# Kernel tuning notes

Measured on AMD Instinct MI355X. Metric: run time of the kernel, lower is better.

The kernel has to match this reference:

```python
import jax, jax.numpy as jnp
import numpy as np

NUM_HEADS = 8
NUM_LANDMARKS = 64


def setup_inputs() -> dict:
    key = jax.random.key(0)
    k1, k2, k3, k4, k5 = jax.random.split(key, 5)
    B, N, C = 4, 8192, 512
    x = jax.random.normal(k1, (B, N, C), dtype=jnp.float32)
    qkv_w = jax.random.normal(k2, (C, 3 * C), dtype=jnp.float32) * (C ** -0.5)
    qkv_b = jax.random.normal(k3, (3 * C,), dtype=jnp.float32) * 0.01
    proj_w = jax.random.normal(k4, (C, C), dtype=jnp.float32) * (C ** -0.5)
    proj_b = jax.random.normal(k5, (C,), dtype=jnp.float32) * 0.01
    return {"x": x, "qkv_w": qkv_w, "qkv_b": qkv_b, "proj_w": proj_w, "proj_b": proj_b}


def reference(x, qkv_w, qkv_b, proj_w, proj_b):
    B, N, C = x.shape
    H = NUM_HEADS
    D = C // H
    m = min(NUM_LANDMARKS, N)
    scale = D ** -0.5

    # qkv projection -> [3, B, H, N, D]
    qkv = (x @ qkv_w + qkv_b).reshape(B, N, 3, H, D).transpose(2, 0, 3, 1, 4)
    q, k, v = qkv[0], qkv[1], qkv[2]

    if m >= N:
        attn = jax.nn.softmax(jnp.einsum('bhnd,bhkd->bhnk', q, k) * scale, axis=-1)
        out = attn @ v  # [B,H,N,D]
    else:
        # landmark indices: linspace(0, N-1, m).long()
        idx = jnp.linspace(0, N - 1, m).astype(jnp.int32)
        q_l = q[:, :, idx]  # [B,H,m,D]
        k_l = k[:, :, idx]  # [B,H,m,D]
        kernel_1 = jax.nn.softmax(jnp.einsum('bhnd,bhmd->bhnm', q, k_l) * scale, axis=-1)  # [B,H,N,m]
        kernel_2 = jax.nn.softmax(jnp.einsum('bhmd,bhkd->bhmk', q_l, k_l) * scale, axis=-1)  # [B,H,m,m]
        kernel_3 = jax.nn.softmax(jnp.einsum('bhmd,bhnd->bhmn', q_l, k) * scale, axis=-1)  # [B,H,m,N]
        k2_inv = jnp.linalg.pinv(kernel_2)  # [B,H,m,m]
        # fuse right-to-left to keep intermediates small: [B,H,m,D]
        out = kernel_1 @ (k2_inv @ (kernel_3 @ v))  # [B,H,N,D]

    out = out.transpose(0, 2, 1, 3).reshape(B, N, C)
    return out @ proj_w + proj_b
```

## Files before the change

### kernel.cpp

```cpp
#include <hip/hip_runtime.h>
#include <stdint.h>

using bf16x8 = __attribute__((ext_vector_type(8))) short;
using bf16x8_t = __attribute__((ext_vector_type(8))) __bf16;
using f32x4  = __attribute__((ext_vector_type(4))) float;
typedef unsigned short u16;
typedef unsigned int   u32;

#define DEVI static __device__ __forceinline__

typedef u32 __attribute__((address_space(1))) gu32;
typedef u32 __attribute__((address_space(3))) lu32;

DEVI u16 f2b(float f) {
  union { float f; u32 u; } v; v.f = f;
  u32 r = v.u + 0x7FFFu + ((v.u >> 16) & 1u);
  return (u16)(r >> 16);
}

DEVI f32x4 mfma16(bf16x8 a, bf16x8 b, f32x4 c) {
  return __builtin_amdgcn_mfma_f32_16x16x32_bf16(
      __builtin_bit_cast(bf16x8_t, a), __builtin_bit_cast(bf16x8_t, b), c, 0, 0, 0);
}

DEVI void gload16(const void* g, void* l) {
  __builtin_amdgcn_global_load_lds((const gu32*)(uintptr_t)g,
                                   (lu32*)(u32)(uintptr_t)l, 16, 0, 0);
}

DEVI int swz64(int row, int ch) { return row*64 + ((ch ^ (row & 7)) << 3); }

#define VMCNT0 asm volatile("s_waitcnt vmcnt(0)" ::: "memory")
#define LGKM0  asm volatile("s_waitcnt lgkmcnt(0)" ::: "memory")

__global__ void __launch_bounds__(256) k_cast_x(const float4* __restrict__ xin,
                                                uint4* __restrict__ xo, int n8) {
  int i = blockIdx.x * 256 + threadIdx.x;
  if (i >= n8) return;
  float4 a = xin[2*i], b = xin[2*i+1];
  uint4 o;
  o.x = ((u32)f2b(a.y) << 16) | f2b(a.x);
  o.y = ((u32)f2b(a.w) << 16) | f2b(a.z);
  o.z = ((u32)f2b(b.y) << 16) | f2b(b.x);
  o.w = ((u32)f2b(b.w) << 16) | f2b(b.z);
  xo[i] = o;
}

__global__ void __launch_bounds__(256) k_tcast(const float* __restrict__ w,
                                               u16* __restrict__ wt, int R, int Cc) {
  int o = blockIdx.x * 256 + threadIdx.x;
  if (o >= R * Cc) return;
  int c = o % R, j = o / R;
  wt[o] = f2b(w[(size_t)c * Cc + j]);
}

__global__ void __launch_bounds__(256) k_lmk(
    const float* __restrict__ x, const float* __restrict__ w,
    const float* __restrict__ bias, float* __restrict__ qlf,
    float* __restrict__ klf, u16* __restrict__ qlb, u16* __restrict__ klb) {
  __shared__ __align__(16) float xr[512];
  const int t = threadIdx.x;
  const int b = blockIdx.x >> 6, i = blockIdx.x & 63;
  const int idx = (i * 8191) / 63;
  const float4* xg = (const float4*)(x + ((size_t)b*8192 + idx)*512);
  if (t < 128) ((float4*)xr)[t] = xg[t];
  __syncthreads();

  const int o0 = t << 2;
  float4 acc = *(const float4*)(bias + o0);
  const float* wp = w + o0;
  #pragma unroll 8
  for (int c = 0; c < 512; ++c) {
    const float xv = xr[c];
    const float4 wv = *(const float4*)(wp + (size_t)c*1536);
    acc.x = fmaf(xv, wv.x, acc.x); acc.y = fmaf(xv, wv.y, acc.y);
    acc.z = fmaf(xv, wv.z, acc.z); acc.w = fmaf(xv, wv.w, acc.w);
  }

  const int h = (o0 >> 6) & 7, d = o0 & 63;
  const size_t ofs = ((size_t)(b*8 + h)*64 + i)*64 + d;
  ushort4 pk;
  pk.x = f2b(acc.x); pk.y = f2b(acc.y); pk.z = f2b(acc.z); pk.w = f2b(acc.w);
  if (o0 < 512) { *(float4*)(qlf + ofs) = acc; *(ushort4*)(qlb + ofs) = pk; }
  else          { *(float4*)(klf + ofs) = acc; *(ushort4*)(klb + ofs) = pk; }
}

template <int MODE>
__global__ void __launch_bounds__(256) k_gemm(
    const u16* __restrict__ A, const u16* __restrict__ Bt,
    const float* __restrict__ bias, int K, int ntn,
    u16* __restrict__ qdst, u16* __restrict__ kdst, u16* __restrict__ vtdst,
    float* __restrict__ fout, int Nout) {
  __shared__ __align__(16) u16 As[128*64];
  __shared__ __align__(16) u16 Bs[128*64];
  const int t = threadIdx.x;
  const int cpx = gridDim.x >> 3;
  const int wgid = (blockIdx.x & 7) * cpx + (blockIdx.x >> 3);
  const int tn = wgid % ntn, tm = wgid / ntn;
  const int m0 = tm << 7, n0 = tn << 7;
  const int w = t >> 6, l = t & 63;
  const int wr = (w >> 1) << 6, wc = (w & 1) << 6;
  const int lhi = l >> 4, llo = l & 15;

  f32x4 acc[4][4];
  #pragma unroll
  for (int i = 0; i < 4; ++i)
    #pragma unroll
    for (int j = 0; j < 4; ++j) acc[i][j] = f32x4{0.f,0.f,0.f,0.f};

  const int csw = (((t & 7) ^ ((t >> 3) & 7)) << 3);
  const u16* ga = A  + (size_t)(m0 + (t >> 3)) * K + csw;
  const u16* gb = Bt + (size_t)(n0 + (t >> 3)) * K + csw;
  u16* lA = As + (w << 9);
  u16* lB = Bs + (w << 9);

  for (int kt = 0; kt < K; kt += 64) {
    __syncthreads();
    #pragma unroll
    for (int i = 0; i < 4; ++i) {
      gload16(ga + (size_t)(i*32)*K + kt, lA + i*2048);
      gload16(gb + (size_t)(i*32)*K + kt, lB + i*2048);
    }
    VMCNT0;
    __syncthreads();
    #pragma unroll
    for (int kko = 0; kko < 64; kko += 32) {
      const int kc = kko >> 3;
      bf16x8 av[4], bv[4];
      #pragma unroll
      for (int mi = 0; mi < 4; ++mi)
        av[mi] = *(const bf16x8*)(As + swz64(wr + mi*16 + llo, kc + lhi));
      #pragma unroll
      for (int ni = 0; ni < 4; ++ni)
        bv[ni] = *(const bf16x8*)(Bs + swz64(wc + ni*16 + llo, kc + lhi));
      #pragma unroll
      for (int mi = 0; mi < 4; ++mi)
        #pragma unroll
        for (int ni = 0; ni < 4; ++ni)
          acc[mi][ni] = mfma16(av[mi], bv[ni], acc[mi][ni]);
    }
  }

  #pragma unroll
  for (int ni = 0; ni < 4; ++ni) {
    const int gcol = n0 + wc + ni*16 + llo;
    const float bvv = bias[gcol];
    if (MODE == 0) {
      const int tt = gcol >> 9, h = (gcol >> 6) & 7, d = gcol & 63;
      #pragma unroll
      for (int mi = 0; mi < 4; ++mi) {
        const int grow = m0 + wr + mi*16 + (lhi << 2);
        const int b = grow >> 13, n = grow & 8191;
        const size_t bh = (size_t)(b*8 + h);
        if (tt == 2) {
          ushort4 pk;
          pk.x = f2b(acc[mi][ni][0] + bvv); pk.y = f2b(acc[mi][ni][1] + bvv);
          pk.z = f2b(acc[mi][ni][2] + bvv); pk.w = f2b(acc[mi][ni][3] + bvv);
          *(ushort4*)(vtdst + (bh*64 + d)*8192 + n) = pk;
        } else {
          u16* dst = (tt == 0 ? qdst : kdst) + (bh*8192 + n)*64 + d;
          #pragma unroll
          for (int r = 0; r < 4; ++r) dst[(size_t)r*64] = f2b(acc[mi][ni][r] + bvv);
        }
      }
    } else {
      #pragma unroll
      for (int mi = 0; mi < 4; ++mi) {
        const int grow = m0 + wr + mi*16 + (lhi << 2);
        #pragma unroll
        for (int r = 0; r < 4; ++r)
          fout[(size_t)(grow + r)*Nout + gcol] = acc[mi][ni][r] + bvv;
      }
    }
  }
}

__global__ void __launch_bounds__(256) k_flash3(
    const u16* __restrict__ qlb, const u16* __restrict__ kmat,
    const u16* __restrict__ vt, float* __restrict__ num_part,
    float* __restrict__ den_part) {
  __shared__ __align__(16) u16 QL[64*64];
  __shared__ __align__(16) u16 KT[4][64*64];
  __shared__ __align__(16) u16 VT[4][64*64];
  __shared__ __align__(16) u16 PL[4][64*64];
  const int t = threadIdx.x, w = t >> 6, l = t & 63;
  const int bh = blockIdx.x >> 3, split = blockIdx.x & 7;
  const int lhi = l >> 4, llo = l & 15;
  const int csw = ((l & 7) ^ (l >> 3)) << 3;

  #pragma unroll
  for (int i = 0; i < 2; ++i)
    gload16(qlb + (size_t)bh*4096 + (size_t)((i*256 + (t & ~7)) << 3)
                + (((t & 7) ^ ((t >> 3) & 7)) << 3),
            QL + i*2048 + (w << 9));
  VMCNT0;
  __syncthreads();

  f32x4 oacc[4][4];
  float dacc[4][4];
  #pragma unroll
  for (int a = 0; a < 4; ++a)
    #pragma unroll
    for (int bq = 0; bq < 4; ++bq) { oacc[a][bq] = f32x4{0.f,0.f,0.f,0.f}; dacc[a][bq] = 0.f; }

  const int nb = split << 10;
  u16* lk = KT[w]; u16* lv = VT[w]; u16* lp = PL[w];
  for (int j = 0; j < 4; ++j) {
    const int n0 = nb + ((w + 4*j) << 6);
    const u16* gk = kmat + ((size_t)bh*8192 + n0 + (l >> 3))*64 + csw;
    const u16* gv = vt   + ((size_t)bh*64 + (l >> 3))*8192 + n0 + csw;
    asm volatile("" ::: "memory");
    LGKM0;
    #pragma unroll
    for (int i = 0; i < 8; ++i) {
      gload16(gk + (size_t)(i*8)*64, lk + i*512);
      gload16(gv + (size_t)(i*8)*8192, lv + i*512);
    }
    VMCNT0;

    f32x4 s[4][4];
    #pragma unroll
    for (int qi = 0; qi < 4; ++qi)
      #pragma unroll
      for (int nj = 0; nj < 4; ++nj) s[qi][nj] = f32x4{0.f,0.f,0.f,0.f};
    #pragma unroll
    for (int kko = 0; kko < 64; kko += 32) {
      const int kc = kko >> 3;
      bf16x8 av[4], bv[4];
      #pragma unroll
      for (int qi = 0; qi < 4; ++qi)
        av[qi] = *(const bf16x8*)(QL + swz64(qi*16 + llo, kc + lhi));
      #pragma unroll
      for (int nj = 0; nj < 4; ++nj)
        bv[nj] = *(const bf16x8*)(lk + swz64(nj*16 + llo, kc + lhi));
      #pragma unroll
      for (int qi = 0; qi < 4; ++qi)
        #pragma unroll
        for (int nj = 0; nj < 4; ++nj)
          s[qi][nj] = mfma16(av[qi], bv[nj], s[qi][nj]);
    }
    #pragma unroll
    for (int qi = 0; qi < 4; ++qi) {
      float rs[4] = {0.f, 0.f, 0.f, 0.f};
      #pragma unroll
      for (int nj = 0; nj < 4; ++nj)
        #pragma unroll
        for (int r = 0; r < 4; ++r) {
          float p = __expf(s[qi][nj][r] * 0.125f);
          rs[r] += p;
          const int prow = qi*16 + lhi*4 + r, pcol = nj*16 + llo;
          lp[swz64(prow, pcol >> 3) + (pcol & 7)] = f2b(p);
        }
      #pragma unroll
      for (int r = 0; r < 4; ++r) {
        float v = rs[r];
        v += __shfl_xor(v, 1); v += __shfl_xor(v, 2);
        v += __shfl_xor(v, 4); v += __shfl_xor(v, 8);
        dacc[qi][r] += v;
      }
    }
    LGKM0;
    #pragma unroll
    for (int kko = 0; kko < 64; kko += 32) {
      const int kc = kko >> 3;
      bf16x8 pa[4], vb[4];
      #pragma unroll
      for (int qi = 0; qi < 4; ++qi)
        pa[qi] = *(const bf16x8*)(lp + swz64(qi*16 + llo, kc + lhi));
      #pragma unroll
      for (int dj = 0; dj < 4; ++dj)
        vb[dj] = *(const bf16x8*)(lv + swz64(dj*16 + llo, kc + lhi));
      #pragma unroll
      for (int qi = 0; qi < 4; ++qi)
        #pragma unroll
        for (int dj = 0; dj < 4; ++dj)
          oacc[qi][dj] = mfma16(pa[qi], vb[dj], oacc[qi][dj]);
    }
  }
  const int sw = (split << 2) + w;
  float* np = num_part + ((size_t)bh*32 + sw)*4096;
  #pragma unroll
  for (int qi = 0; qi < 4; ++qi)
    #pragma unroll
    for (int dj = 0; dj < 4; ++dj)
      #pragma unroll
      for (int r = 0; r < 4; ++r)
        np[(qi*16 + lhi*4 + r)*64 + dj*16 + llo] = oacc[qi][dj][r];
  if (llo == 0) {
    float* dp = den_part + ((size_t)bh*32 + sw)*64;
    #pragma unroll
    for (int qi = 0; qi < 4; ++qi)
      #pragma unroll
      for (int r = 0; r < 4; ++r)
        dp[qi*16 + lhi*4 + r] = dacc[qi][r];
  }
}

__global__ void __launch_bounds__(256) k_t1(
    const float* __restrict__ num_part, const float* __restrict__ den_part,
    float* __restrict__ t1g) {
  const int t = threadIdx.x;
  const int bh = blockIdx.x >> 2, ch = blockIdx.x & 3;
  const int f = ch*256 + t;
  const int m = f >> 4;
  const float4* ng = (const float4*)num_part + (size_t)bh*32*1024;
  float4 acc = {0.f, 0.f, 0.f, 0.f};
  float ds = 0.f;
  for (int s = 0; s < 32; ++s) {
    float4 v = ng[(size_t)s*1024 + f];
    acc.x += v.x; acc.y += v.y; acc.z += v.z; acc.w += v.w;
    ds += den_part[((size_t)bh*32 + s)*64 + m];
  }
  float r = 1.f / ds;
  acc.x *= r; acc.y *= r; acc.z *= r; acc.w *= r;
  ((float4*)t1g)[(size_t)bh*1024 + f] = acc;
}

__global__ void __launch_bounds__(256) k_inv(
    const float* __restrict__ qlf, const float* __restrict__ klf,
    float* __restrict__ invg) {
  __shared__ __align__(16) float A[64*132];
  __shared__ __align__(16) float QL[64*68], KL[64*68];
  __shared__ int pivcol[64];
  __shared__ int piv_s;
  const int t = threadIdx.x;
  const int bh = blockIdx.x;
  const int i4 = t >> 2, jc = t & 3;
  float4* QL4 = (float4*)QL;
  float4* KL4 = (float4*)KL;
  float4* A4  = (float4*)A;

  const float4* qg = (const float4*)(qlf + (size_t)bh*4096);
  const float4* kg = (const float4*)(klf + (size_t)bh*4096);
  #pragma unroll
  for (int k = 0; k < 4; ++k) {
    int g = k*256 + t, row = g >> 4, c4 = g & 15;
    QL4[row*17 + c4] = qg[g];
    KL4[row*17 + c4] = kg[g];
  }
  __syncthreads();

  {
    float4 qreg[16];
    #pragma unroll
    for (int q4 = 0; q4 < 16; ++q4) qreg[q4] = QL4[i4*17 + q4];
    #pragma unroll
    for (int jj = 0; jj < 16; ++jj) {
      int j = jc*16 + jj;
      float acc = 0.f;
      #pragma unroll
      for (int q4 = 0; q4 < 16; ++q4) {
        float4 kv = KL4[j*17 + q4];
        acc = fmaf(qreg[q4].x, kv.x, acc); acc = fmaf(qreg[q4].y, kv.y, acc);
        acc = fmaf(qreg[q4].z, kv.z, acc); acc = fmaf(qreg[q4].w, kv.w, acc);
      }
      A[i4*132 + j] = acc * 0.125f;
    }
  }
  {
    float z[16]; float m = -1e30f;
    #pragma unroll
    for (int jj = 0; jj < 16; ++jj) { z[jj] = A[i4*132 + jc*16 + jj]; m = fmaxf(m, z[jj]); }
    m = fmaxf(m, __shfl_xor(m, 1)); m = fmaxf(m, __shfl_xor(m, 2));
    float s = 0.f;
    #pragma unroll
    for (int jj = 0; jj < 16; ++jj) { z[jj] = __expf(z[jj] - m); s += z[jj]; }
    s += __shfl_xor(s, 1); s += __shfl_xor(s, 2);
    float rinv = 1.f / s;
    #pragma unroll
    for (int jj = 0; jj < 16; ++jj) {
      int j = jc*16 + jj;
      A[i4*132 + j] = z[jj] * rinv;
      A[i4*132 + 64 + j] = (j == i4) ? 1.f : 0.f;
    }
  }
  __syncthreads();

  const int r = i4, q = jc;
  int used = 0;
  for (int c = 0; c < 64; ++c) {
    if (t < 64) {
      float val = used ? -1.f : fabsf(A[t*132 + c]);
      int idx = t;
      #pragma unroll
      for (int mk = 1; mk < 64; mk <<= 1) {
        float ov = __shfl_xor(val, mk);
        int oi = __shfl_xor(idx, mk);
        int take = (ov > val) || (ov == val && oi < idx);
        val = take ? ov : val;
        idx = take ? oi : idx;
      }
      if (t == idx) { used = 1; pivcol[t] = c; }
      if (t == 0) piv_s = idx;
    }
    __syncthreads();
    const int p = piv_s;
    if (r != p) {
      const float coef = -A[r*132 + c] / A[p*132 + c];
      const float4* Ap = A4 + p*33 + q*8;
      float4* Ar = A4 + r*33 + q*8;
      #pragma unroll
      for (int i = 0; i < 8; ++i) {
        float4 a = Ar[i], pv = Ap[i];
        a.x = fmaf(coef, pv.x, a.x); a.y = fmaf(coef, pv.y, a.y);
        a.z = fmaf(coef, pv.z, a.z); a.w = fmaf(coef, pv.w, a.w);
        Ar[i] = a;
      }
    }
    __syncthreads();
  }

  {
    const int cr = pivcol[r];
    const float rd = 1.f / A[r*132 + cr];
    float4* og = (float4*)(invg + (size_t)bh*4096 + (size_t)cr*64) + q*4;
    #pragma unroll
    for (int i = 0; i < 4; ++i) {
      float4 v = A4[r*33 + 16 + q*4 + i];
      v.x *= rd; v.y *= rd; v.z *= rd; v.w *= rd;
      og[i] = v;
    }
  }
}

__global__ void __launch_bounds__(256) k_t2(
    const float* __restrict__ invg, const float* __restrict__ t1g,
    float* __restrict__ t2t) {
  __shared__ __align__(16) float IV[64*68];
  __shared__ __align__(16) float T1[64*68];
  const int t = threadIdx.x;
  const int bh = blockIdx.x;
  const int i4 = t >> 2, jc = t & 3;
  float4* IV4 = (float4*)IV;
  float4* T14 = (float4*)T1;
  const float4* ig = (const float4*)(invg + (size_t)bh*4096);
  const float4* tg = (const float4*)(t1g + (size_t)bh*4096);
  #pragma unroll
  for (int k = 0; k < 4; ++k) {
    int g = k*256 + t, row = g >> 4, c4 = g & 15;
    IV4[row*17 + c4] = ig[g];
    T14[row*17 + c4] = tg[g];
  }
  __syncthreads();
  float acc[16];
  #pragma unroll
  for (int d = 0; d < 16; ++d) acc[d] = 0.f;
  for (int m = 0; m < 64; ++m) {
    float wv = IV[i4*68 + m];
    #pragma unroll
    for (int d4 = 0; d4 < 4; ++d4) {
      float4 tv = T14[m*17 + jc*4 + d4];
      acc[d4*4+0] = fmaf(wv, tv.x, acc[d4*4+0]);
      acc[d4*4+1] = fmaf(wv, tv.y, acc[d4*4+1]);
      acc[d4*4+2] = fmaf(wv, tv.z, acc[d4*4+2]);
      acc[d4*4+3] = fmaf(wv, tv.w, acc[d4*4+3]);
    }
  }
  #pragma unroll
  for (int dd = 0; dd < 16; ++dd) {
    int d = jc*16 + dd;
    t2t[((size_t)bh*64 + d)*64 + i4] = acc[dd];
  }
}

__global__ void __launch_bounds__(256) k_flash1(
    const u16* __restrict__ q, const u16* __restrict__ klb,
    const float* __restrict__ t2t, u16* __restrict__ oatt) {
  __shared__ __align__(16) u16 KL[64*64];
  __shared__ __align__(16) u16 T2[64*64];
  __shared__ __align__(16) u16 QT[4][64*64];
  __shared__ __align__(16) u16 PL[4][64*64];
  const int t = threadIdx.x, w = t >> 6, l = t & 63;
  const int bh = blockIdx.x >> 5, blk = blockIdx.x & 31;
  const int lhi = l >> 4, llo = l & 15;
  const int b = bh >> 3, h = bh & 7;
  const int csw = ((l & 7) ^ (l >> 3)) << 3;

  #pragma unroll
  for (int i = 0; i < 2; ++i)
    gload16(klb + (size_t)bh*4096 + (size_t)((i*256 + (t & ~7)) << 3)
                + (((t & 7) ^ ((t >> 3) & 7)) << 3),
            KL + i*2048 + (w << 9));
  for (int i = t; i < 4096; i += 256)
    T2[swz64(i >> 6, (i & 63) >> 3) + (i & 7)] = f2b(t2t[(size_t)bh*4096 + i]);
  VMCNT0;
  __syncthreads();

  const int n0 = (blk << 8) + (w << 6);
  const u16* gq = q + ((size_t)bh*8192 + n0 + (l >> 3))*64 + csw;
  u16* lq = QT[w]; u16* lp = PL[w];
  #pragma unroll
  for (int i = 0; i < 8; ++i) gload16(gq + (size_t)(i*8)*64, lq + i*512);
  VMCNT0;

  f32x4 s[4][4];
  #pragma unroll
  for (int qi = 0; qi < 4; ++qi)
    #pragma unroll
    for (int nj = 0; nj < 4; ++nj) s[qi][nj] = f32x4{0.f,0.f,0.f,0.f};
  #pragma unroll
  for (int kko = 0; kko < 64; kko += 32) {
    const int kc = kko >> 3;
    bf16x8 av[4], bv[4];
    #pragma unroll
    for (int qi = 0; qi < 4; ++qi)
      av[qi] = *(const bf16x8*)(lq + swz64(qi*16 + llo, kc + lhi));
    #pragma unroll
    for (int nj = 0; nj < 4; ++nj)
      bv[nj] = *(const bf16x8*)(KL + swz64(nj*16 + llo, kc + lhi));
    #pragma unroll
    for (int qi = 0; qi < 4; ++qi)
      #pragma unroll
      for (int nj = 0; nj < 4; ++nj)
        s[qi][nj] = mfma16(av[qi], bv[nj], s[qi][nj]);
  }
  float rcp_[4][4];
  #pragma unroll
  for (int qi = 0; qi < 4; ++qi) {
    float mx[4] = {-1e30f, -1e30f, -1e30f, -1e30f};
    #pragma unroll
    for (int nj = 0; nj < 4; ++nj)
      #pragma unroll
      for (int r = 0; r < 4; ++r) {
        float z = s[qi][nj][r] * 0.125f;
        s[qi][nj][r] = z;
        mx[r] = fmaxf(mx[r], z);
      }
    #pragma unroll
    for (int r = 0; r < 4; ++r) {
      float m = mx[r];
      m = fmaxf(m, __shfl_xor(m, 1)); m = fmaxf(m, __shfl_xor(m, 2));
      m = fmaxf(m, __shfl_xor(m, 4)); m = fmaxf(m, __shfl_xor(m, 8));
      mx[r] = m;
    }
    float rs[4] = {0.f, 0.f, 0.f, 0.f};
    #pragma unroll
    for (int nj = 0; nj < 4; ++nj)
      #pragma unroll
      for (int r = 0; r < 4; ++r) {
        float p = __expf(s[qi][nj][r] - mx[r]);
        rs[r] += p;
        const int prow = qi*16 + lhi*4 + r, pcol = nj*16 + llo;
        lp[swz64(prow, pcol >> 3) + (pcol & 7)] = f2b(p);
      }
    #pragma unroll
    for (int r = 0; r < 4; ++r) {
      float v = rs[r];
      v += __shfl_xor(v, 1); v += __shfl_xor(v, 2);
      v += __shfl_xor(v, 4); v += __shfl_xor(v, 8);
      rcp_[qi][r] = 1.0f / v;
    }
  }
  LGKM0;
  f32x4 o[4][4];
  #pragma unroll
  for (int qi = 0; qi < 4; ++qi)
    #pragma unroll
    for (int dj = 0; dj < 4; ++dj) o[qi][dj] = f32x4{0.f,0.f,0.f,0.f};
  #pragma unroll
  for (int kko = 0; kko < 64; kko += 32) {
    const int kc = kko >> 3;
    bf16x8 pa[4], tb[4];
    #pragma unroll
    for (int qi = 0; qi < 4; ++qi)
      pa[qi] = *(const bf16x8*)(lp + swz64(qi*16 + llo, kc + lhi));
    #pragma unroll
    for (int dj = 0; dj < 4; ++dj)
      tb[dj] = *(const bf16x8*)(T2 + swz64(dj*16 + llo, kc + lhi));
    #pragma unroll
    for (int qi = 0; qi < 4; ++qi)
      #pragma unroll
      for (int dj = 0; dj < 4; ++dj)
        o[qi][dj] = mfma16(pa[qi], tb[dj], o[qi][dj]);
  }
  #pragma unroll
  for (int qi = 0; qi < 4; ++qi)
    #pragma unroll
    for (int dj = 0; dj < 4; ++dj)
      #pragma unroll
      for (int r = 0; r < 4; ++r) {
        int n = n0 + qi*16 + lhi*4 + r;
        oatt[((size_t)b*8192 + n)*512 + h*64 + dj*16 + llo] = f2b(o[qi][dj][r] * rcp_[qi][r]);
      }
}

extern "C" void kernel_launch(void* const* d_in, const int* in_sizes, int n_in,
                              void* d_out, int out_size, void* d_ws, size_t ws_size,
                              hipStream_t stream) {
  const float* x      = (const float*)d_in[0];
  const float* qkv_w  = (const float*)d_in[1];
  const float* qkv_b  = (const float*)d_in[2];
  const float* proj_w = (const float*)d_in[3];
  const float* proj_b = (const float*)d_in[4];
  float* out = (float*)d_out;

  char* ws = (char*)d_ws;
  size_t off = 0;
  auto alloc = [&](size_t bytes) -> char* {
    char* p = ws + off;
    off += (bytes + 255) & ~(size_t)255;
    return p;
  };
  u16*   x_bf  = (u16*)  alloc(33554432);
  u16*   vt    = (u16*)  alloc(33554432);
  u16*   wqkvt = (u16*)  alloc(1572864);
  u16*   wprjt = (u16*)  alloc(524288);
  float* qlf   = (float*)alloc(524288);
  float* klf   = (float*)alloc(524288);
  u16*   qlb   = (u16*)  alloc(262144);
  u16*   klb   = (u16*)  alloc(262144);
  float* nump  = (float*)alloc(16777216);
  float* denp  = (float*)alloc(262144);
  float* t2t   = (float*)alloc(524288);
  float* t1g   = (float*)alloc(524288);
  float* invg  = (float*)alloc(524288);
  if (off > ws_size) return;

  u16* qm   = (u16*)d_out;
  u16* kmat = qm + 16777216;
  u16* oatt = x_bf;

  k_cast_x<<<8192, 256, 0, stream>>>((const float4*)x, (uint4*)x_bf, 2097152);
  k_tcast<<<3072, 256, 0, stream>>>(qkv_w, wqkvt, 512, 1536);
  k_tcast<<<1024, 256, 0, stream>>>(proj_w, wprjt, 512, 512);
  k_lmk<<<256, 256, 0, stream>>>(x, qkv_w, qkv_b, qlf, klf, qlb, klb);
  k_gemm<0><<<3072, 256, 0, stream>>>(x_bf, wqkvt, qkv_b, 512, 12, qm, kmat, vt, nullptr, 0);
  k_flash3<<<256, 256, 0, stream>>>(qlb, kmat, vt, nump, denp);
  k_t1<<<128, 256, 0, stream>>>(nump, denp, t1g);
  k_inv<<<32, 256, 0, stream>>>(qlf, klf, invg);
  k_t2<<<32, 256, 0, stream>>>(invg, t1g, t2t);
  k_flash1<<<1024, 256, 0, stream>>>(qm, klb, t2t, oatt);
  k_gemm<1><<<1024, 256, 0, stream>>>(oatt, wprjt, proj_b, 512, 4, nullptr, nullptr, nullptr, out, 512);
}
```

Measured before the change: 315.5 us.

## Fold landmark pseudo-inverse into QKV GEMM launch as extra workgroups

Removes the standalone k_inv launch and runs the 64x64 softmax-plus-Gauss-Jordan inversion inside k_gemm<0>, using 32 extra workgroups that branch off before the GEMM path. The serial, sync-heavy inversion then overlaps with the large QKV GEMM instead of running on only 32 blocks by itself, and one kernel launch goes away. The GEMM now uses a shared char buffer sized for the larger inversion scratch, which raises its LDS footprint slightly. The tile index mapping also shifts because the grid size changes, which may alter cache locality.

```diff
diff --git a/kernel.cpp b/kernel.cpp
--- a/kernel.cpp
+++ b/kernel.cpp
@@ -90,13 +90,122 @@
     const u16* __restrict__ A, const u16* __restrict__ Bt,
     const float* __restrict__ bias, int K, int ntn,
     u16* __restrict__ qdst, u16* __restrict__ kdst, u16* __restrict__ vtdst,
-    float* __restrict__ fout, int Nout) {
-  __shared__ __align__(16) u16 As[128*64];
-  __shared__ __align__(16) u16 Bs[128*64];
+    float* __restrict__ fout, int Nout,
+    const float* __restrict__ qlf, const float* __restrict__ klf,
+    float* __restrict__ invg) {
+  constexpr int SMEM_BYTES = (MODE == 0) ? 34064 : 32768;
+  __shared__ __align__(16) char smem[SMEM_BYTES];
   const int t = threadIdx.x;
   const int cpx = gridDim.x >> 3;
   const int wgid = (blockIdx.x & 7) * cpx + (blockIdx.x >> 3);
-  const int tn = wgid % ntn, tm = wgid / ntn;
+
+  if (MODE == 0 && wgid < 32) {
+    float* Am = (float*)smem;
+    int* pivcol = (int*)(smem + 33792);
+    int* piv_sp = (int*)(smem + 33792 + 256);
+    float4* A4 = (float4*)Am;
+    const int bh = wgid;
+    const int i4 = t >> 2, jc = t & 3;
+
+    const float4* kg = (const float4*)(klf + (size_t)bh*4096);
+    for (int g = t; g < 1024; g += 256) {
+      int j = g >> 4, d4 = g & 15;
+      ((float4*)(Am + j*132 + 64))[d4] = kg[g];
+    }
+    __syncthreads();
+
+    {
+      float4 qreg[16];
+      const float4* qg = (const float4*)(qlf + (size_t)bh*4096 + (size_t)i4*64);
+      #pragma unroll
+      for (int q4 = 0; q4 < 16; ++q4) qreg[q4] = qg[q4];
+      #pragma unroll
+      for (int jj = 0; jj < 16; ++jj) {
+        int j = jc*16 + jj;
+        const float4* kv4 = (const float4*)(Am + j*132 + 64);
+        float acc = 0.f;
+        #pragma unroll
+        for (int q4 = 0; q4 < 16; ++q4) {
+          float4 kv = kv4[q4];
+          acc = fmaf(qreg[q4].x, kv.x, acc); acc = fmaf(qreg[q4].y, kv.y, acc);
+          acc = fmaf(qreg[q4].z, kv.z, acc); acc = fmaf(qreg[q4].w, kv.w, acc);
+        }
+        Am[i4*132 + j] = acc * 0.125f;
+      }
+    }
+    __syncthreads();
+
+    {
+      float z[16]; float m = -1e30f;
+      #pragma unroll
+      for (int jj = 0; jj < 16; ++jj) { z[jj] = Am[i4*132 + jc*16 + jj]; m = fmaxf(m, z[jj]); }
+      m = fmaxf(m, __shfl_xor(m, 1)); m = fmaxf(m, __shfl_xor(m, 2));
+      float s = 0.f;
+      #pragma unroll
+      for (int jj = 0; jj < 16; ++jj) { z[jj] = __expf(z[jj] - m); s += z[jj]; }
+      s += __shfl_xor(s, 1); s += __shfl_xor(s, 2);
+      float rinv = 1.f / s;
+      #pragma unroll
+      for (int jj = 0; jj < 16; ++jj) {
+        int j = jc*16 + jj;
+        Am[i4*132 + j] = z[jj] * rinv;
+        Am[i4*132 + 64 + j] = (j == i4) ? 1.f : 0.f;
+      }
+    }
+    __syncthreads();
+
+    const int r = i4, q = jc;
+    int used = 0;
+    for (int c = 0; c < 64; ++c) {
+      if (t < 64) {
+        float val = used ? -1.f : fabsf(Am[t*132 + c]);
+        int idx = t;
+        #pragma unroll
+        for (int mk = 1; mk < 64; mk <<= 1) {
+          float ov = __shfl_xor(val, mk);
+          int oi = __shfl_xor(idx, mk);
+          int take = (ov > val) || (ov == val && oi < idx);
+          val = take ? ov : val;
+          idx = take ? oi : idx;
+        }
+        if (t == idx) { used = 1; pivcol[t] = c; }
+        if (t == 0) *piv_sp = idx;
+      }
+      __syncthreads();
+      const int p = *piv_sp;
+      if (r != p) {
+        const float coef = -Am[r*132 + c] / Am[p*132 + c];
+        const float4* Ap = A4 + p*33 + q*8;
+        float4* Ar = A4 + r*33 + q*8;
+        #pragma unroll
+        for (int i = 0; i < 8; ++i) {
+          float4 a = Ar[i], pv = Ap[i];
+          a.x = fmaf(coef, pv.x, a.x); a.y = fmaf(coef, pv.y, a.y);
+          a.z = fmaf(coef, pv.z, a.z); a.w = fmaf(coef, pv.w, a.w);
+          Ar[i] = a;
+        }
+      }
+      __syncthreads();
+    }
+
+    {
+      const int cr = pivcol[r];
+      const float rd = 1.f / Am[r*132 + cr];
+      float4* og = (float4*)(invg + (size_t)bh*4096 + (size_t)cr*64) + q*4;
+      #pragma unroll
+      for (int i = 0; i < 4; ++i) {
+        float4 v = A4[r*33 + 16 + q*4 + i];
+        v.x *= rd; v.y *= rd; v.z *= rd; v.w *= rd;
+        og[i] = v;
+      }
+    }
+    return;
+  }
+
+  u16* As = (u16*)smem;
+  u16* Bs = (u16*)(smem + 16384);
+  const int wg2 = wgid - (MODE == 0 ? 32 : 0);
+  const int tn = wg2 % ntn, tm = wg2 / ntn;
   const int m0 = tm << 7, n0 = tn << 7;
   const int w = t >> 6, l = t & 63;
   const int wr = (w >> 1) << 6, wc = (w & 1) << 6;
@@ -314,113 +423,6 @@
   float r = 1.f / ds;
   acc.x *= r; acc.y *= r; acc.z *= r; acc.w *= r;
   ((float4*)t1g)[(size_t)bh*1024 + f] = acc;
-}
-
-__global__ void __launch_bounds__(256) k_inv(
-    const float* __restrict__ qlf, const float* __restrict__ klf,
-    float* __restrict__ invg) {
-  __shared__ __align__(16) float A[64*132];
-  __shared__ __align__(16) float QL[64*68], KL[64*68];
-  __shared__ int pivcol[64];
-  __shared__ int piv_s;
-  const int t = threadIdx.x;
-  const int bh = blockIdx.x;
-  const int i4 = t >> 2, jc = t & 3;
-  float4* QL4 = (float4*)QL;
-  float4* KL4 = (float4*)KL;
-  float4* A4  = (float4*)A;
-
-  const float4* qg = (const float4*)(qlf + (size_t)bh*4096);
-  const float4* kg = (const float4*)(klf + (size_t)bh*4096);
-  #pragma unroll
-  for (int k = 0; k < 4; ++k) {
-    int g = k*256 + t, row = g >> 4, c4 = g & 15;
-    QL4[row*17 + c4] = qg[g];
-    KL4[row*17 + c4] = kg[g];
-  }
-  __syncthreads();
-
-  {
-    float4 qreg[16];
-    #pragma unroll
-    for (int q4 = 0; q4 < 16; ++q4) qreg[q4] = QL4[i4*17 + q4];
-    #pragma unroll
-    for (int jj = 0; jj < 16; ++jj) {
-      int j = jc*16 + jj;
-      float acc = 0.f;
-      #pragma unroll
-      for (int q4 = 0; q4 < 16; ++q4) {
-        float4 kv = KL4[j*17 + q4];
-        acc = fmaf(qreg[q4].x, kv.x, acc); acc = fmaf(qreg[q4].y, kv.y, acc);
-        acc = fmaf(qreg[q4].z, kv.z, acc); acc = fmaf(qreg[q4].w, kv.w, acc);
-      }
-      A[i4*132 + j] = acc * 0.125f;
-    }
-  }
-  {
-    float z[16]; float m = -1e30f;
-    #pragma unroll
-    for (int jj = 0; jj < 16; ++jj) { z[jj] = A[i4*132 + jc*16 + jj]; m = fmaxf(m, z[jj]); }
-    m = fmaxf(m, __shfl_xor(m, 1)); m = fmaxf(m, __shfl_xor(m, 2));
-    float s = 0.f;
-    #pragma unroll
-    for (int jj = 0; jj < 16; ++jj) { z[jj] = __expf(z[jj] - m); s += z[jj]; }
-    s += __shfl_xor(s, 1); s += __shfl_xor(s, 2);
-    float rinv = 1.f / s;
-    #pragma unroll
-    for (int jj = 0; jj < 16; ++jj) {
-      int j = jc*16 + jj;
-      A[i4*132 + j] = z[jj] * rinv;
-      A[i4*132 + 64 + j] = (j == i4) ? 1.f : 0.f;
-    }
-  }
-  __syncthreads();
-
-  const int r = i4, q = jc;
-  int used = 0;
-  for (int c = 0; c < 64; ++c) {
-    if (t < 64) {
-      float val = used ? -1.f : fabsf(A[t*132 + c]);
-      int idx = t;
-      #pragma unroll
-      for (int mk = 1; mk < 64; mk <<= 1) {
-        float ov = __shfl_xor(val, mk);
-        int oi = __shfl_xor(idx, mk);
-        int take = (ov > val) || (ov == val && oi < idx);
-        val = take ? ov : val;
-        idx = take ? oi : idx;
-      }
-      if (t == idx) { used = 1; pivcol[t] = c; }
-      if (t == 0) piv_s = idx;
-    }
-    __syncthreads();
-    const int p = piv_s;
-    if (r != p) {
-      const float coef = -A[r*132 + c] / A[p*132 + c];
-      const float4* Ap = A4 + p*33 + q*8;
-      float4* Ar = A4 + r*33 + q*8;
-      #pragma unroll
-      for (int i = 0; i < 8; ++i) {
-        float4 a = Ar[i], pv = Ap[i];
-        a.x = fmaf(coef, pv.x, a.x); a.y = fmaf(coef, pv.y, a.y);
-        a.z = fmaf(coef, pv.z, a.z); a.w = fmaf(coef, pv.w, a.w);
-        Ar[i] = a;
-      }
-    }
-    __syncthreads();
-  }
-
-  {
-    const int cr = pivcol[r];
-    const float rd = 1.f / A[r*132 + cr];
-    float4* og = (float4*)(invg + (size_t)bh*4096 + (size_t)cr*64) + q*4;
-    #pragma unroll
-    for (int i = 0; i < 4; ++i) {
-      float4 v = A4[r*33 + 16 + q*4 + i];
-      v.x *= rd; v.y *= rd; v.z *= rd; v.w *= rd;
-      og[i] = v;
-    }
-  }
 }
 
 __global__ void __launch_bounds__(256) k_t2(
@@ -624,11 +626,12 @@
   k_tcast<<<3072, 256, 0, stream>>>(qkv_w, wqkvt, 512, 1536);
   k_tcast<<<1024, 256, 0, stream>>>(proj_w, wprjt, 512, 512);
   k_lmk<<<256, 256, 0, stream>>>(x, qkv_w, qkv_b, qlf, klf, qlb, klb);
-  k_gemm<0><<<3072, 256, 0, stream>>>(x_bf, wqkvt, qkv_b, 512, 12, qm, kmat, vt, nullptr, 0);
+  k_gemm<0><<<3104, 256, 0, stream>>>(x_bf, wqkvt, qkv_b, 512, 12, qm, kmat, vt,
+                                      nullptr, 0, qlf, klf, invg);
   k_flash3<<<256, 256, 0, stream>>>(qlb, kmat, vt, nump, denp);
   k_t1<<<128, 256, 0, stream>>>(nump, denp, t1g);
-  k_inv<<<32, 256, 0, stream>>>(qlf, klf, invg);
   k_t2<<<32, 256, 0, stream>>>(invg, t1g, t2t);
   k_flash1<<<1024, 256, 0, stream>>>(qm, klb, t2t, oatt);
-  k_gemm<1><<<1024, 256, 0, stream>>>(oatt, wprjt, proj_b, 512, 4, nullptr, nullptr, nullptr, out, 512);
-}
+  k_gemm<1><<<1024, 256, 0, stream>>>(oatt, wprjt, proj_b, 512, 4, nullptr, nullptr,
+                                      nullptr, out, 512, nullptr, nullptr, nullptr);
+}
```

Result: faster. 273.4 us, median of 3 (-13.4%).
